# Kernel tuning notes

Hardware: AMD Instinct MI355X
Metric: run time of the kernel (lower is better)

## Reference

```python
import jax, jax.numpy as jnp
import numpy as np

HIDDEN = 2048
NUM_HEADS = 16
NUM_KV_HEADS = 8
HEAD_DIM = 128
EPS = 1e-6
ROPE_THETA = 10000.0
Q_SIZE = NUM_HEADS * HEAD_DIM
KV_SIZE = NUM_KV_HEADS * HEAD_DIM


def setup_inputs() -> dict:
    key = jax.random.key(0)
    k1, k2, k3 = jax.random.split(key, 3)
    B, S = 2, 2048
    positions = jnp.broadcast_to(jnp.arange(S, dtype=jnp.int32), (B, S))
    hidden_states = jax.random.normal(k1, (B, S, HIDDEN), dtype=jnp.float32)
    w_qkv = jax.random.normal(k2, (Q_SIZE + 2 * KV_SIZE, HIDDEN), dtype=jnp.float32) * (HIDDEN ** -0.5)
    w_o = jax.random.normal(k3, (HIDDEN, Q_SIZE), dtype=jnp.float32) * (Q_SIZE ** -0.5)
    q_norm_w = jnp.ones((HEAD_DIM,), dtype=jnp.float32)
    k_norm_w = jnp.ones((HEAD_DIM,), dtype=jnp.float32)
    return {"positions": positions, "hidden_states": hidden_states,
            "w_qkv": w_qkv, "w_o": w_o, "q_norm_w": q_norm_w, "k_norm_w": k_norm_w}


def _rms_norm(x, w):
    # x: [..., HEAD_DIM]
    var = jnp.mean(x * x, axis=-1, keepdims=True)
    return x * jax.lax.rsqrt(var + EPS) * w


def _rope(x, cos, sin):
    # x: [B, S, H, D]; cos/sin: [B, S, 1, D/2] (neox style: rotate half)
    x1, x2 = jnp.split(x, 2, axis=-1)
    return jnp.concatenate([x1 * cos - x2 * sin, x2 * cos + x1 * sin], axis=-1)


def reference(positions, hidden_states, w_qkv, w_o, q_norm_w, k_norm_w):
    B, S, _ = hidden_states.shape
    qkv = jnp.einsum("bsh,oh->bso", hidden_states, w_qkv)
    q, k, v = jnp.split(qkv, [Q_SIZE, Q_SIZE + KV_SIZE], axis=-1)
    q = q.reshape(B, S, NUM_HEADS, HEAD_DIM)
    k = k.reshape(B, S, NUM_KV_HEADS, HEAD_DIM)
    v = v.reshape(B, S, NUM_KV_HEADS, HEAD_DIM)

    # per-head RMSNorm on q and k (Qwen3 qk-norm)
    q = _rms_norm(q, q_norm_w)
    k = _rms_norm(k, k_norm_w)

    # RoPE (neox style)
    inv_freq = 1.0 / (ROPE_THETA ** (jnp.arange(0, HEAD_DIM, 2, dtype=jnp.float32) / HEAD_DIM))
    angles = positions.astype(jnp.float32)[..., None] * inv_freq  # [B, S, D/2]
    cos = jnp.cos(angles)[:, :, None, :]
    sin = jnp.sin(angles)[:, :, None, :]
    q = _rope(q, cos, sin)
    k = _rope(k, cos, sin)

    # GQA: expand kv heads to match q heads
    rep = NUM_HEADS // NUM_KV_HEADS
    k = jnp.repeat(k, rep, axis=2)  # [B, S, H, D]
    v = jnp.repeat(v, rep, axis=2)

    scale = HEAD_DIM ** -0.5
    scores = jnp.einsum("bqhd,bkhd->bhqk", q, k) * scale
    causal = jnp.tril(jnp.ones((S, S), dtype=bool))
    scores = jnp.where(causal, scores, jnp.finfo(scores.dtype).min)
    probs = jax.nn.softmax(scores, axis=-1)
    attn = jnp.einsum("bhqk,bkhd->bqhd", probs, v).reshape(B, S, Q_SIZE)
    return jnp.einsum("bso,ho->bsh", attn, w_o)
```

## Files before the change

### kernel.cpp

```cpp
#include <hip/hip_runtime.h>
#include <hip/hip_bf16.h>
#include <cstdint>
#include <cstddef>

#define HIDDEN 2048
#define NHEADS 16
#define NKV    8
#define HD     128
#define QS     (NHEADS*HD)
#define KVS    (NKV*HD)
#define OC     (QS + 2*KVS)
#define BB     2
#define SS     2048
#define ROWS   (BB*SS)

typedef __bf16 bf16;
typedef __bf16 bf16x8 __attribute__((ext_vector_type(8)));
typedef __bf16 bf16x4 __attribute__((ext_vector_type(4)));
typedef float  f32x4  __attribute__((ext_vector_type(4)));
typedef float  f32x2  __attribute__((ext_vector_type(2)));
typedef float  f32x16 __attribute__((ext_vector_type(16)));
typedef int    i32x4  __attribute__((ext_vector_type(4)));

__device__ __forceinline__ float fexp2(float x) {
#if __has_builtin(__builtin_amdgcn_exp2f)
  return __builtin_amdgcn_exp2f(x);
#else
  return __expf(x * 0.6931471805599453f);
#endif
}

__global__ __launch_bounds__(256) void k_cvt(const float* __restrict__ src,
                                             bf16* __restrict__ dst, int n8) {
  int i = blockIdx.x * blockDim.x + threadIdx.x;
  int stride = gridDim.x * blockDim.x;
  for (; i < n8; i += stride) {
    const f32x4* s = (const f32x4*)(src + (size_t)i * 8);
    f32x4 a = s[0], b = s[1];
    bf16x8 o;
    o[0]=(bf16)a[0]; o[1]=(bf16)a[1]; o[2]=(bf16)a[2]; o[3]=(bf16)a[3];
    o[4]=(bf16)b[0]; o[5]=(bf16)b[1]; o[6]=(bf16)b[2]; o[7]=(bf16)b[3];
    *(bf16x8*)(dst + (size_t)i * 8) = o;
  }
}

__global__ __launch_bounds__(256) void k_cvt2(const float* __restrict__ s0, bf16* __restrict__ d0, int n0,
                                              const float* __restrict__ s1, bf16* __restrict__ d1, int n1) {
  int i = blockIdx.x * blockDim.x + threadIdx.x;
  int stride = gridDim.x * blockDim.x;
  int total = n0 + n1;
  for (; i < total; i += stride) {
    const float* src; bf16* dst; int k;
    if (i < n0) { src = s0; dst = d0; k = i; }
    else        { src = s1; dst = d1; k = i - n0; }
    const f32x4* s = (const f32x4*)(src + (size_t)k * 8);
    f32x4 a = s[0], b = s[1];
    bf16x8 o;
    o[0]=(bf16)a[0]; o[1]=(bf16)a[1]; o[2]=(bf16)a[2]; o[3]=(bf16)a[3];
    o[4]=(bf16)b[0]; o[5]=(bf16)b[1]; o[6]=(bf16)b[2]; o[7]=(bf16)b[3];
    *(bf16x8*)(dst + (size_t)k * 8) = o;
  }
}

__global__ __launch_bounds__(256) void k_table(float* __restrict__ tbl) {
  int t = blockIdx.x * blockDim.x + threadIdx.x;
  int pos = t >> 6, i = t & 63;
  float freq = powf(10000.0f, -(float)i / 64.0f);
  float ang = (float)pos * freq;
  float sv, cv;
  sincosf(ang, &sv, &cv);
  f32x2 v; v[0] = cv; v[1] = sv;
  ((f32x2*)tbl)[t] = v;
}

__device__ __forceinline__ void gll16(const void* g, void* l) {
  __builtin_amdgcn_global_load_lds((const __attribute__((address_space(1))) void*)g,
                                   (__attribute__((address_space(3))) void*)l, 16, 0, 0);
}

template <typename OT>
__global__ __launch_bounds__(256) void k_gemm(const bf16* __restrict__ A,
                                              const bf16* __restrict__ Bw,
                                              OT* __restrict__ C,
                                              int M, int N, int K) {
  const int tid = threadIdx.x;
  const int lane = tid & 63;
  const int w = tid >> 6;
  const int H = blockIdx.x + gridDim.x * blockIdx.y;
  const int cpx = (gridDim.x * gridDim.y) >> 3;
  const int swz = (H & 7) * cpx + (H >> 3);
  const int bx = swz % gridDim.x, by = swz / gridDim.x;
  const int m0 = by * 128, n0 = bx * 128;
  __shared__ bf16 As[128 * 64];
  __shared__ bf16 Bs[128 * 64];
  f32x16 acc[2][2] = {};
  const int wm = (w >> 1) * 64, wn = (w & 1) * 64;
  const int l31 = lane & 31, hg = lane >> 5;
  const int rgA = (w >> 1) * 2;
  const int rgB = (w & 1) * 2;
  const int KT = K >> 6;
  for (int kt = 0; kt < KT; ++kt) {
    __syncthreads();
    #pragma unroll
    for (int i = 0; i < 4; ++i) {
      int c = tid + i * 256;
      int hg_  = c & 1;
      int l31_ = (c >> 1) & 31;
      int s_   = (c >> 6) & 3;
      int rg_  = c >> 8;
      size_t soff = (size_t)(rg_ * 32 + l31_) * K + kt * 64 + s_ * 16 + hg_ * 8;
      gll16(A + (size_t)m0 * K + soff, As + (size_t)(c & ~63) * 8);
      gll16(Bw + (size_t)n0 * K + soff, Bs + (size_t)(c & ~63) * 8);
    }
    asm volatile("s_waitcnt vmcnt(0)" ::: "memory");
    __syncthreads();
    bf16x8 af[2][4], bfv[2][4];
    #pragma unroll
    for (int i = 0; i < 2; ++i)
      #pragma unroll
      for (int s = 0; s < 4; ++s)
        af[i][s] = *(const bf16x8*)((char*)As + (((rgA + i) * 4 + s) * 1024 + l31 * 32 + hg * 16));
    #pragma unroll
    for (int j = 0; j < 2; ++j)
      #pragma unroll
      for (int s = 0; s < 4; ++s)
        bfv[j][s] = *(const bf16x8*)((char*)Bs + (((rgB + j) * 4 + s) * 1024 + l31 * 32 + hg * 16));
    #pragma unroll
    for (int i = 0; i < 2; ++i)
      #pragma unroll
      for (int j = 0; j < 2; ++j)
        #pragma unroll
        for (int s = 0; s < 4; ++s)
          acc[i][j] = __builtin_amdgcn_mfma_f32_32x32x16_bf16(af[i][s], bfv[j][s], acc[i][j], 0, 0, 0);
  }
  #pragma unroll
  for (int i = 0; i < 2; ++i)
    #pragma unroll
    for (int j = 0; j < 2; ++j) {
      int col = n0 + wn + j * 32 + l31;
      #pragma unroll
      for (int reg = 0; reg < 16; ++reg) {
        int row = m0 + wm + i * 32 + 4 * hg + (reg & 3) + 8 * (reg >> 2);
        C[(size_t)row * N + col] = (OT)acc[i][j][reg];
      }
    }
}

__global__ __launch_bounds__(256) void k_ropenorm(const bf16* __restrict__ qkv,
                                                  bf16* __restrict__ qb, bf16* __restrict__ kb,
                                                  const float* __restrict__ tbl,
                                                  const int* __restrict__ pos,
                                                  const float* __restrict__ qw,
                                                  const float* __restrict__ kw) {
  int gw = blockIdx.x * 4 + (threadIdx.x >> 6);
  int lane = threadIdx.x & 63;
  int h = gw % 24;
  int rem = gw / 24;
  int s = rem & (SS - 1);
  int b = rem >> 11;
  size_t row = (size_t)b * SS + s;
  int col0 = (h < 16) ? h * HD : QS + (h - 16) * HD;
  unsigned u = *(const unsigned*)(qkv + row * OC + col0 + lane * 2);
  float x0 = __uint_as_float((u & 0xffffu) << 16);
  float x1 = __uint_as_float(u & 0xffff0000u);
  float ssq = x0 * x0 + x1 * x1;
  for (int m = 1; m < 64; m <<= 1) ssq += __shfl_xor(ssq, m, 64);
  float r = rsqrtf(ssq * (1.0f / 128.0f) + 1e-6f);
  const float* wv = (h < 16) ? qw : kw;
  float y0 = x0 * r * wv[lane * 2], y1 = x1 * r * wv[lane * 2 + 1];
  float p0 = __shfl_xor(y0, 32, 64), p1 = __shfl_xor(y1, 32, 64);
  int p = pos[row];
  f32x4 cs = *(const f32x4*)(tbl + (size_t)p * 128 + (lane & 31) * 4);
  float o0, o1;
  if (lane < 32) { o0 = y0 * cs[0] - p0 * cs[1]; o1 = y1 * cs[2] - p1 * cs[3]; }
  else           { o0 = y0 * cs[0] + p0 * cs[1]; o1 = y1 * cs[2] + p1 * cs[3]; }
  bf16* dst; size_t drow;
  if (h < 16) {
    const float scl2 = 0.12753102f;
    o0 *= scl2; o1 *= scl2;
    dst = qb; drow = ((size_t)b * NHEADS + h) * SS + s;
  } else {
    dst = kb; drow = ((size_t)b * NKV + (h - 16)) * SS + s;
  }
  bf16 v0 = (bf16)o0, v1 = (bf16)o1;
  unsigned short q0, q1;
  __builtin_memcpy(&q0, &v0, 2); __builtin_memcpy(&q1, &v1, 2);
  *(unsigned*)(dst + drow * HD + lane * 2) = (unsigned)q0 | ((unsigned)q1 << 16);
}

__global__ __launch_bounds__(256) void k_vt(const bf16* __restrict__ qkv,
                                            bf16* __restrict__ vT) {
  __shared__ bf16 T[64 * 136];
  int tid = threadIdx.x;
  int st = blockIdx.x, kv = blockIdx.y, b = blockIdx.z;
  int s0 = st * 64;
  for (int i = 0; i < 4; ++i) {
    int c = tid + i * 256;
    int sl = c >> 4, dc = c & 15;
    i32x4 v = *(const i32x4*)(qkv + (size_t)(b * SS + s0 + sl) * OC + QS + KVS + kv * HD + dc * 8);
    *(i32x4*)(T + sl * 136 + dc * 8) = v;
  }
  __syncthreads();
  for (int i = 0; i < 4; ++i) {
    int c = tid + i * 256;
    int d = c >> 3, sg = c & 7;
    bf16x8 o;
    for (int j = 0; j < 8; ++j) o[j] = T[(sg * 8 + j) * 136 + d];
    *(bf16x8*)(vT + ((size_t)(b * NKV + kv) * HD + d) * SS + s0 + sg * 8) = o;
  }
}

__global__ __launch_bounds__(256) void k_attn9(const bf16* __restrict__ qb,
                                               const bf16* __restrict__ kb,
                                               const bf16* __restrict__ vT,
                                               bf16* __restrict__ out) {
  __shared__ bf16 Kl[64 * 128];
  __shared__ bf16 Vl[128 * 64];
  __shared__ bf16 Pl[4][16 * 64];
  const int tid = threadIdx.x, lane = tid & 63, w = tid >> 6;
  const int L = blockIdx.x + 32 * (blockIdx.y + 16 * blockIdx.z);
  const int r8 = L & 7;
  const int c4 = (L >> 3) & 3;
  const int i32_ = L >> 5;
  const int g = r8 * 4 + c4;
  const int h = g >> 1, b = g & 1;
  const int a_ = i32_ & 7, m_ = i32_ >> 3;
  const int qt = (m_ == 0) ? a_ : (m_ == 1) ? (15 - a_) : (m_ == 2) ? (16 + a_) : (31 - a_);
  const int kvh = h >> 1;
  const int lr = lane & 15, lg = lane >> 4;
  const int qbase = qt * 64 + w * 16;
  const float NEG = -3.0e38f;
  bf16x8 qf[4];
  {
    const bf16* qrow = qb + ((size_t)(b * NHEADS + h) * SS + qbase + lr) * HD;
    #pragma unroll
    for (int ks = 0; ks < 4; ++ks) qf[ks] = *(const bf16x8*)(qrow + ks * 32 + lg * 8);
  }
  f32x4 acc[8] = {};
  float m_r = NEG, l_r = 0.0f;
  const bf16* Kg = kb + (size_t)(b * NKV + kvh) * SS * HD;
  const bf16* Vg = vT + (size_t)(b * NKV + kvh) * HD * SS;
  for (int t = 0; t <= qt; ++t) {
    const int kv0 = t * 64;
    __syncthreads();
    #pragma unroll
    for (int i = 0; i < 4; ++i) {
      int c = tid + i * 256;
      int r_ = c >> 4;
      int ch = (c & 15) ^ (r_ & 7);
      gll16(Kg + (size_t)(kv0 + r_) * HD + ch * 8, Kl + (size_t)(c & ~63) * 8);
    }
    #pragma unroll
    for (int i = 0; i < 4; ++i) {
      int c = tid + i * 256;
      int d = c >> 3;
      int ch = (c & 7) ^ (d & 7);
      gll16(Vg + (size_t)d * SS + kv0 + ch * 8, Vl + (size_t)(c & ~63) * 8);
    }
    asm volatile("s_waitcnt vmcnt(0)" ::: "memory");
    __syncthreads();
    f32x4 sf[4];
    __builtin_amdgcn_s_setprio(1);
    #pragma unroll
    for (int mt = 0; mt < 4; ++mt) {
      f32x4 a2 = {0.f, 0.f, 0.f, 0.f};
      const int rrow = mt * 16 + lr;
      #pragma unroll
      for (int ks = 0; ks < 4; ++ks) {
        bf16x8 kf = *(const bf16x8*)((char*)Kl + ((rrow * 256 + ks * 64 + lg * 16) ^ ((rrow & 7) << 4)));
        a2 = __builtin_amdgcn_mfma_f32_16x16x32_bf16(kf, qf[ks], a2, 0, 0, 0);
      }
      sf[mt] = a2;
    }
    __builtin_amdgcn_s_setprio(0);
    const int qg = qbase + lr;
    float pm = NEG;
    if (t == qt) {
      #pragma unroll
      for (int mt = 0; mt < 4; ++mt)
        #pragma unroll
        for (int r = 0; r < 4; ++r) {
          int kvg = kv0 + mt * 16 + lg * 4 + r;
          float v = sf[mt][r];
          if (kvg > qg) v = NEG;
          sf[mt][r] = v;
          pm = fmaxf(pm, v);
        }
    } else {
      #pragma unroll
      for (int mt = 0; mt < 4; ++mt)
        #pragma unroll
        for (int r = 0; r < 4; ++r) pm = fmaxf(pm, sf[mt][r]);
    }
    pm = fmaxf(pm, __shfl_xor(pm, 16, 64));
    pm = fmaxf(pm, __shfl_xor(pm, 32, 64));
    if (!__all(pm <= m_r + 11.5415603f)) {
      const float mn = fmaxf(m_r, pm);
      const float scale = fexp2(m_r - mn);
      float sr[4];
      #pragma unroll
      for (int r = 0; r < 4; ++r) sr[r] = __shfl(scale, lg * 4 + r, 64);
      #pragma unroll
      for (int nt = 0; nt < 8; ++nt)
        #pragma unroll
        for (int r = 0; r < 4; ++r) acc[nt][r] *= sr[r];
      l_r *= scale;
      m_r = mn;
    }
    float ts = 0.f;
    #pragma unroll
    for (int mt = 0; mt < 4; ++mt)
      #pragma unroll
      for (int r = 0; r < 4; ++r) {
        float pv = fexp2(sf[mt][r] - m_r);
        sf[mt][r] = pv;
        ts += pv;
      }
    ts += __shfl_xor(ts, 16, 64);
    ts += __shfl_xor(ts, 32, 64);
    l_r += ts;
    #pragma unroll
    for (int mt = 0; mt < 4; ++mt) {
      bf16x4 pk;
      #pragma unroll
      for (int r = 0; r < 4; ++r) pk[r] = (bf16)sf[mt][r];
      *(bf16x4*)((char*)&Pl[w][0] + ((lr * 128 + mt * 32 + lg * 8) ^ ((lr & 7) << 4))) = pk;
    }
    __builtin_amdgcn_s_setprio(1);
    #pragma unroll
    for (int kk = 0; kk < 2; ++kk) {
      bf16x8 pa = *(const bf16x8*)((char*)&Pl[w][0] + ((lr * 128 + kk * 64 + lg * 16) ^ ((lr & 7) << 4)));
      #pragma unroll
      for (int nt = 0; nt < 8; ++nt) {
        const int d = nt * 16 + lr;
        bf16x8 vbf = *(const bf16x8*)((char*)Vl + ((d * 128 + kk * 64 + lg * 16) ^ ((d & 7) << 4)));
        acc[nt] = __builtin_amdgcn_mfma_f32_16x16x32_bf16(pa, vbf, acc[nt], 0, 0, 0);
      }
    }
    __builtin_amdgcn_s_setprio(0);
  }
  const float inv = 1.0f / l_r;
  float ir[4];
  #pragma unroll
  for (int r = 0; r < 4; ++r) ir[r] = __shfl(inv, lg * 4 + r, 64);
  #pragma unroll
  for (int nt = 0; nt < 8; ++nt)
    #pragma unroll
    for (int r = 0; r < 4; ++r) {
      size_t row = (size_t)b * SS + qbase + lg * 4 + r;
      out[row * QS + h * HD + nt * 16 + lr] = (bf16)(acc[nt][r] * ir[r]);
    }
}

extern "C" void kernel_launch(void* const* d_in, const int* in_sizes, int n_in,
                              void* d_out, int out_size, void* d_ws, size_t ws_size,
                              hipStream_t stream) {
  const int*   pos  = (const int*)d_in[0];
  const float* hid  = (const float*)d_in[1];
  const float* wqkv = (const float*)d_in[2];
  const float* wo   = (const float*)d_in[3];
  const float* qw   = (const float*)d_in[4];
  const float* kw   = (const float*)d_in[5];
  char* ws = (char*)d_ws;
  bf16* hid_bf  = (bf16*)(ws + 0);
  bf16* attn_o  = hid_bf;
  bf16* wqkv_bf = (bf16*)(ws + 16777216);
  bf16* q_buf   = wqkv_bf;
  bf16* k_buf   = (bf16*)(ws + 33554432);
  bf16* wo_bf   = k_buf;
  bf16* qkv     = (bf16*)(ws + 41943040);
  bf16* vT      = (bf16*)(ws + 75497472);
  float* tbl    = (float*)(ws + 83886080);

  k_cvt2<<<dim3(2048), dim3(256), 0, stream>>>(
      hid, hid_bf, ROWS * HIDDEN / 8,
      wqkv, wqkv_bf, OC * HIDDEN / 8);
  k_table<<<dim3(512), dim3(256), 0, stream>>>(tbl);
  k_gemm<bf16><<<dim3(OC / 128, ROWS / 128), dim3(256), 0, stream>>>(
      hid_bf, wqkv_bf, qkv, ROWS, OC, HIDDEN);
  k_ropenorm<<<dim3(ROWS * 24 / 4), dim3(256), 0, stream>>>(
      qkv, q_buf, k_buf, tbl, pos, qw, kw);
  k_vt<<<dim3(SS / 64, NKV, BB), dim3(256), 0, stream>>>(qkv, vT);
  k_attn9<<<dim3(SS / 64, NHEADS, BB), dim3(256), 0, stream>>>(
      q_buf, k_buf, vT, attn_o);
  k_cvt<<<dim3(2048), dim3(256), 0, stream>>>(wo, wo_bf, HIDDEN * QS / 8);
  k_gemm<float><<<dim3(HIDDEN / 128, ROWS / 128), dim3(256), 0, stream>>>(
      attn_o, wo_bf, (float*)d_out, ROWS, HIDDEN, QS);
}
```

Baseline: 270.6 us.

## Pre-tile GEMM operands into contiguous LDS-order blocks during conversion

The fp32-to-bf16 conversion kernels now write the hidden states and weights in a blocked layout, with each 128x64 tile stored contiguously in the exact order the GEMM's global-to-LDS loads consume it. The attention epilogue writes its output straight into the same blocked layout so it can feed the output projection GEMM. The GEMM's per-chunk address arithmetic collapses to a contiguous offset, and each wave's loads become fully sequential instead of strided rows. In exchange the conversion kernels read with a strided pattern, the attention output stores are scattered, and the GEMM now only works for operands laid out this way (K fixed at 2048 in the converter).

```diff
diff --git a/kernel.cpp b/kernel.cpp
--- a/kernel.cpp
+++ b/kernel.cpp
@@ -30,35 +30,46 @@
 #endif
 }
 
-__global__ __launch_bounds__(256) void k_cvt(const float* __restrict__ src,
-                                             bf16* __restrict__ dst, int n8) {
-  int i = blockIdx.x * blockDim.x + threadIdx.x;
+
+__global__ __launch_bounds__(256) void k_cvtb(const float* __restrict__ src,
+                                              bf16* __restrict__ dst, int nchunks) {
+  int G = blockIdx.x * blockDim.x + threadIdx.x;
   int stride = gridDim.x * blockDim.x;
-  for (; i < n8; i += stride) {
-    const f32x4* s = (const f32x4*)(src + (size_t)i * 8);
-    f32x4 a = s[0], b = s[1];
+  for (; G < nchunks; G += stride) {
+    int c = G & 1023, tile = G >> 10;
+    int P = tile >> 5, kt = tile & 31;
+    int hg = c & 1, l31 = (c >> 1) & 31, s = (c >> 6) & 3, rg = c >> 8;
+    int row = P * 128 + rg * 32 + l31;
+    int k = kt * 64 + s * 16 + hg * 8;
+    const f32x4* sp = (const f32x4*)(src + (size_t)row * 2048 + k);
+    f32x4 a = sp[0], b2 = sp[1];
     bf16x8 o;
     o[0]=(bf16)a[0]; o[1]=(bf16)a[1]; o[2]=(bf16)a[2]; o[3]=(bf16)a[3];
-    o[4]=(bf16)b[0]; o[5]=(bf16)b[1]; o[6]=(bf16)b[2]; o[7]=(bf16)b[3];
-    *(bf16x8*)(dst + (size_t)i * 8) = o;
-  }
-}
-
-__global__ __launch_bounds__(256) void k_cvt2(const float* __restrict__ s0, bf16* __restrict__ d0, int n0,
-                                              const float* __restrict__ s1, bf16* __restrict__ d1, int n1) {
-  int i = blockIdx.x * blockDim.x + threadIdx.x;
+    o[4]=(bf16)b2[0]; o[5]=(bf16)b2[1]; o[6]=(bf16)b2[2]; o[7]=(bf16)b2[3];
+    *(bf16x8*)(dst + (size_t)G * 8) = o;
+  }
+}
+
+__global__ __launch_bounds__(256) void k_cvtb2(const float* __restrict__ s0, bf16* __restrict__ d0, int n0,
+                                               const float* __restrict__ s1, bf16* __restrict__ d1, int n1) {
+  int G = blockIdx.x * blockDim.x + threadIdx.x;
   int stride = gridDim.x * blockDim.x;
   int total = n0 + n1;
-  for (; i < total; i += stride) {
-    const float* src; bf16* dst; int k;
-    if (i < n0) { src = s0; dst = d0; k = i; }
-    else        { src = s1; dst = d1; k = i - n0; }
-    const f32x4* s = (const f32x4*)(src + (size_t)k * 8);
-    f32x4 a = s[0], b = s[1];
+  for (; G < total; G += stride) {
+    const float* src; bf16* dst; int g;
+    if (G < n0) { src = s0; dst = d0; g = G; }
+    else        { src = s1; dst = d1; g = G - n0; }
+    int c = g & 1023, tile = g >> 10;
+    int P = tile >> 5, kt = tile & 31;
+    int hg = c & 1, l31 = (c >> 1) & 31, s = (c >> 6) & 3, rg = c >> 8;
+    int row = P * 128 + rg * 32 + l31;
+    int k = kt * 64 + s * 16 + hg * 8;
+    const f32x4* sp = (const f32x4*)(src + (size_t)row * 2048 + k);
+    f32x4 a = sp[0], b2 = sp[1];
     bf16x8 o;
     o[0]=(bf16)a[0]; o[1]=(bf16)a[1]; o[2]=(bf16)a[2]; o[3]=(bf16)a[3];
-    o[4]=(bf16)b[0]; o[5]=(bf16)b[1]; o[6]=(bf16)b[2]; o[7]=(bf16)b[3];
-    *(bf16x8*)(dst + (size_t)k * 8) = o;
+    o[4]=(bf16)b2[0]; o[5]=(bf16)b2[1]; o[6]=(bf16)b2[2]; o[7]=(bf16)b2[3];
+    *(bf16x8*)(dst + (size_t)g * 8) = o;
   }
 }
 
@@ -101,16 +112,13 @@
   const int KT = K >> 6;
   for (int kt = 0; kt < KT; ++kt) {
     __syncthreads();
+    const size_t tA = ((size_t)((m0 >> 7) * KT + kt)) << 13;
+    const size_t tB = ((size_t)((n0 >> 7) * KT + kt)) << 13;
     #pragma unroll
     for (int i = 0; i < 4; ++i) {
       int c = tid + i * 256;
-      int hg_  = c & 1;
-      int l31_ = (c >> 1) & 31;
-      int s_   = (c >> 6) & 3;
-      int rg_  = c >> 8;
-      size_t soff = (size_t)(rg_ * 32 + l31_) * K + kt * 64 + s_ * 16 + hg_ * 8;
-      gll16(A + (size_t)m0 * K + soff, As + (size_t)(c & ~63) * 8);
-      gll16(Bw + (size_t)n0 * K + soff, Bs + (size_t)(c & ~63) * 8);
+      gll16(A + tA + (size_t)c * 8, As + (size_t)(c & ~63) * 8);
+      gll16(Bw + tB + (size_t)c * 8, Bs + (size_t)(c & ~63) * 8);
     }
     asm volatile("s_waitcnt vmcnt(0)" ::: "memory");
     __syncthreads();
@@ -343,13 +351,21 @@
   float ir[4];
   #pragma unroll
   for (int r = 0; r < 4; ++r) ir[r] = __shfl(inv, lg * 4 + r, 64);
+  const int hgE = (lr >> 3) & 1, eE = lr & 7;
   #pragma unroll
-  for (int nt = 0; nt < 8; ++nt)
+  for (int nt = 0; nt < 8; ++nt) {
+    const int ktE = h * 2 + (nt >> 2);
+    const int sE = nt & 3;
     #pragma unroll
     for (int r = 0; r < 4; ++r) {
-      size_t row = (size_t)b * SS + qbase + lg * 4 + r;
-      out[row * QS + h * HD + nt * 16 + lr] = (bf16)(acc[nt][r] * ir[r]);
-    }
+      int rowi = b * SS + qbase + lg * 4 + r;
+      int P = rowi >> 7, rr = rowi & 127;
+      int rg = rr >> 5, l31r = rr & 31;
+      int cE = ((rg * 4 + sE) * 32 + l31r) * 2 + hgE;
+      size_t addr = (((size_t)(P * 32 + ktE)) << 13) + (size_t)cE * 8 + eE;
+      out[addr] = (bf16)(acc[nt][r] * ir[r]);
+    }
+  }
 }
 
 extern "C" void kernel_launch(void* const* d_in, const int* in_sizes, int n_in,
@@ -372,7 +388,7 @@
   bf16* vT      = (bf16*)(ws + 75497472);
   float* tbl    = (float*)(ws + 83886080);
 
-  k_cvt2<<<dim3(2048), dim3(256), 0, stream>>>(
+  k_cvtb2<<<dim3(2048), dim3(256), 0, stream>>>(
       hid, hid_bf, ROWS * HIDDEN / 8,
       wqkv, wqkv_bf, OC * HIDDEN / 8);
   k_table<<<dim3(512), dim3(256), 0, stream>>>(tbl);
@@ -383,7 +399,7 @@
   k_vt<<<dim3(SS / 64, NKV, BB), dim3(256), 0, stream>>>(qkv, vT);
   k_attn9<<<dim3(SS / 64, NHEADS, BB), dim3(256), 0, stream>>>(
       q_buf, k_buf, vT, attn_o);
-  k_cvt<<<dim3(2048), dim3(256), 0, stream>>>(wo, wo_bf, HIDDEN * QS / 8);
+  k_cvtb<<<dim3(2048), dim3(256), 0, stream>>>(wo, wo_bf, HIDDEN * QS / 8);
   k_gemm<float><<<dim3(HIDDEN / 128, ROWS / 128), dim3(256), 0, stream>>>(
       attn_o, wo_bf, (float*)d_out, ROWS, HIDDEN, QS);
 }
```

New measurement: 272.8 us. No clear change (+0.8%).
